# Kernel optimization log

Hardware: AMD Instinct MI355X
Metric: run time of the kernel (lower is better)

Reference implementation:

```python
import jax, jax.numpy as jnp
import numpy as np
import math

B, C, L = 64, 16, 4096
EMB, DEPTH, NEXP = 256, 2, 4
SHAPE, STRIDE = 8, 4
NPATCH = (L - SHAPE) // STRIDE + 1  # 1023
SPARSE = 0.5
NF = 32

def gelu(x):
    return jax.nn.gelu(x, approximate=False)

def conv1d(x, w, stride=1, pad=0):
    return jax.lax.conv_general_dilated(x, w, (stride,), [(pad, pad)],
                                        dimension_numbers=('NCH', 'OIH', 'NCH'))

def rmsnorm(x, g):
    # F.normalize(x, dim=-1) * gamma * sqrt(D)
    n = jnp.sqrt(jnp.sum(x * x, axis=-1, keepdims=True))
    return x / jnp.maximum(n, 1e-12) * g * (x.shape[-1] ** 0.5)

def setup_inputs():
    ks = jax.random.split(jax.random.key(0), 16)
    r = lambda i, s: jax.random.normal(ks[i], s, jnp.float32) * 0.02
    return dict(
        x=jax.random.normal(ks[0], (B, C, L), jnp.float32),
        epoch=100, warm_up=50,
        emb_w=r(1, (EMB, C, SHAPE)), emb_b=jnp.zeros((EMB,), jnp.float32),
        pos_embed=r(2, (1, NPATCH, EMB)),
        attn_w1=r(3, (EMB, 8)), attn_b1=jnp.zeros((8,), jnp.float32),
        attn_w2=r(4, (8, 1)), attn_b2=jnp.zeros((1,), jnp.float32),
        gate_w=r(5, (EMB, NEXP)), gate_b=jnp.zeros((NEXP,), jnp.float32),
        ex_w1=r(6, (NEXP, EMB, EMB)), ex_b1=jnp.zeros((NEXP, EMB), jnp.float32),
        ex_w2=r(7, (NEXP, EMB, EMB)), ex_b2=jnp.zeros((NEXP, EMB), jnp.float32),
        moe_gamma=jnp.ones((EMB,), jnp.float32),
        norm1_g=jnp.ones((DEPTH, EMB), jnp.float32),
        norm2_g=jnp.ones((DEPTH, EMB), jnp.float32),
        bott_w=r(8, (DEPTH, NF, EMB, 1)),
        conv_w39=r(9, (DEPTH, NF, NF, 39)),
        conv_w19=r(10, (DEPTH, NF, NF, 19)),
        conv_w9=r(11, (DEPTH, NF, NF, 9)),
        mp_w=r(12, (DEPTH, NF, EMB, 1)),
        bn_g=jnp.ones((DEPTH, 4 * NF), jnp.float32),
        bn_b=jnp.zeros((DEPTH, 4 * NF), jnp.float32),
        proj_w=r(13, (DEPTH, 4 * NF, EMB)),
        proj_b=jnp.zeros((DEPTH, EMB), jnp.float32),
        head_w=r(14, (EMB, 1)), head_b=jnp.zeros((1,), jnp.float32),
    )

def _forward(x, epoch, warm_up, emb_w, emb_b, pos_embed, attn_w1, attn_b1,
             attn_w2, attn_b2, gate_w, gate_b, ex_w1, ex_b1, ex_w2, ex_b2,
             moe_gamma, norm1_g, norm2_g, bott_w, conv_w39, conv_w19, conv_w9,
             mp_w, bn_g, bn_b, proj_w, proj_b, head_w, head_b):
    def attn(h):  # (B,N,D) -> (B,N,1) sigmoid importance scores
        return jax.nn.sigmoid(jnp.tanh(h @ attn_w1 + attn_b1) @ attn_w2 + attn_b2)

    def moe(h):  # top-1 routed MoE; compute all experts densely, select via one-hot
        Bm, Nm, D = h.shape
        hf = h.reshape(-1, D)  # (T, D)
        logits = jax.nn.softmax(hf @ gate_w + gate_b, axis=-1)  # (T, E)
        top_idx = jnp.argmax(logits, axis=-1)
        top_val = jnp.max(logits, axis=-1, keepdims=True)
        mid = gelu(jnp.einsum('td,edh->eth', hf, ex_w1) + ex_b1[:, None, :])
        ye = jnp.einsum('eth,ehd->etd', mid, ex_w2) + ex_b2[:, None, :]
        sel = jax.nn.one_hot(top_idx, NEXP, dtype=h.dtype)  # (T, E)
        out = jnp.einsum('etd,te->td', ye, sel)
        y = rmsnorm((hf + out * top_val).reshape(Bm, Nm, D), moe_gamma)
        imp = logits.sum(0)
        load = jnp.var(imp, ddof=1) / (imp.mean() ** 2 + 1e-10)
        return gelu(y), load

    def inception(xc, i):  # xc: (B, D, T) -> (B, 4*NF, T)
        xb = conv1d(xc, bott_w[i])  # bottleneck 1x1 -> NF channels
        mp = jax.lax.reduce_window(xc, -jnp.inf, jax.lax.max, (1, 1, 3),
                                   (1, 1, 1), [(0, 0), (0, 0), (1, 1)])
        out = jnp.concatenate([conv1d(xb, conv_w39[i], pad=19),
                               conv1d(xb, conv_w19[i], pad=9),
                               conv1d(xb, conv_w9[i], pad=4),
                               conv1d(mp, mp_w[i])], axis=1)
        # BatchNorm1d eval mode: running mean 0 / var 1, affine gamma/beta
        out = out * (bn_g[i] / np.float32(np.sqrt(1.0 + 1e-5)))[None, :, None] \
              + bn_b[i][None, :, None]
        return gelu(out)

    def incep_branch(h, i):  # (B,N,D) -> (B,N,D)
        io = inception(jnp.transpose(h, (0, 2, 1)), i)
        return jnp.transpose(io, (0, 2, 1)) @ proj_w[i] + proj_b[i]

    h = conv1d(x, emb_w, stride=STRIDE) + emb_b[None, :, None]  # (B, EMB, N)
    h = jnp.transpose(h, (0, 2, 1)) + pos_embed  # N == NPATCH -> no interp
    # pos_drop is identity at inference

    schedule = np.linspace(0.0, SPARSE, DEPTH)
    total_loss = jnp.zeros((), h.dtype)
    end_scores = None
    for i in range(DEPTH):
        ratio = 1.0 if epoch < warm_up else 1.0 - float(schedule[i])
        is_last = (i == DEPTH - 1)
        N = h.shape[1]
        x_n = rmsnorm(h, norm1_g[i])
        scores = attn(x_n)  # (B, N, 1)
        if ratio < 1.0 and N > 2:
            left_k = max(math.ceil(ratio * N), 1)
            xs = x_n * scores
            idx = jnp.sort(jax.lax.top_k(scores[..., 0], left_k)[1], axis=1)
            left_x = jnp.take_along_axis(xs, idx[:, :, None], axis=1)
            # sum of non-topk tokens == total sum minus topk sum
            extra = xs.sum(1, keepdims=True) - left_x.sum(1, keepdims=True)
            h = jnp.concatenate([left_x, extra], axis=1)  # (B, left_k+1, D)
            x_n2 = rmsnorm(h, norm2_g[i])
            moe_out, loss = moe(x_n2)
            h = h + moe_out + incep_branch(x_n2, i)
            total_loss = total_loss + loss
        else:
            h = x_n * scores
            h = h + incep_branch(rmsnorm(h, norm2_g[i]), i)
        if is_last:
            end_scores = attn(h)  # dropout identity; scores on pre-gelu x
        h = gelu(h)
    logits = h @ head_w + head_b  # (B, N', 1)
    cls = (logits * end_scores).mean(axis=1)  # (B, 1)
    return cls[..., 0], total_loss

def reference(x, epoch, warm_up, emb_w, emb_b, pos_embed, attn_w1, attn_b1,
              attn_w2, attn_b2, gate_w, gate_b, ex_w1, ex_b1, ex_w2, ex_b2,
              moe_gamma, norm1_g, norm2_g, bott_w, conv_w39, conv_w19, conv_w9,
              mp_w, bn_g, bn_b, proj_w, proj_b, head_w, head_b):
    return _forward(x, epoch, warm_up, emb_w, emb_b, pos_embed, attn_w1,
                    attn_b1, attn_w2, attn_b2, gate_w, gate_b, ex_w1, ex_b1,
                    ex_w2, ex_b2, moe_gamma, norm1_g, norm2_g, bott_w,
                    conv_w39, conv_w19, conv_w9, mp_w, bn_g, bn_b, proj_w,
                    proj_b, head_w, head_b)
```

## Files before the change

kernel.cpp:

```cpp
#include <hip/hip_runtime.h>
#include <math.h>

#define BB 64
#define EMB 256
#define N0 1023
#define N1 513
#define NTOK0 (BB * N0)
#define NTOK1 (BB * N1)
#define GCH 16

typedef __attribute__((ext_vector_type(8))) short short8;
typedef __attribute__((ext_vector_type(4))) float f32x4;

__device__ __forceinline__ float gelu_f(float x) {
    return 0.5f * x * (1.0f + erff(x * 0.7071067811865476f));
}

__device__ __forceinline__ float4 gelu4(float4 v) {
    return make_float4(gelu_f(v.x), gelu_f(v.y), gelu_f(v.z), gelu_f(v.w));
}

__device__ __forceinline__ float wave_reduce(float v) {
#pragma unroll
    for (int o = 32; o > 0; o >>= 1) v += __shfl_down(v, o, 64);
    return v;
}

__device__ __forceinline__ float attn_finish(float p[8], const float* __restrict__ b1,
                                             const float* __restrict__ w2, float b2v,
                                             int lane) {
#pragma unroll
    for (int o = 1; o <= 4; o <<= 1) {
#pragma unroll
        for (int j = 0; j < 8; j++) p[j] += __shfl_xor(p[j], o, 64);
    }
    int j = lane & 7;
    float a0 = (j & 1) ? p[1] : p[0];
    float a1 = (j & 1) ? p[3] : p[2];
    float a2 = (j & 1) ? p[5] : p[4];
    float a3 = (j & 1) ? p[7] : p[6];
    float c0 = (j & 2) ? a1 : a0;
    float c1 = (j & 2) ? a3 : a2;
    float q  = (j & 4) ? c1 : c0;
#pragma unroll
    for (int o = 8; o <= 32; o <<= 1) q += __shfl_xor(q, o, 64);
    float w = tanhf(q + b1[j]) * w2[j];
#pragma unroll
    for (int o = 1; o <= 4; o <<= 1) w += __shfl_xor(w, o, 64);
    float z = w + b2v;
    return 1.0f / (1.0f + expf(-z));
}

__device__ __forceinline__ unsigned short f2bf(float f) {
    unsigned int u = __float_as_uint(f);
    u = (u + 0x7FFFu + ((u >> 16) & 1u)) >> 16;
    return (unsigned short)u;
}
__device__ __forceinline__ float bf2f(unsigned short h) {
    return __uint_as_float(((unsigned int)h) << 16);
}

__global__ void convert_bf16(const float* __restrict__ ew1, const float* __restrict__ ew2,
                             const float* __restrict__ pjw,
                             const float* __restrict__ cw39, const float* __restrict__ cw19,
                             const float* __restrict__ cw9, const float* __restrict__ embw,
                             const float* __restrict__ bott, const float* __restrict__ mpw,
                             unsigned short* __restrict__ w1t, unsigned short* __restrict__ w2t,
                             unsigned short* __restrict__ pjwb,
                             unsigned short* __restrict__ cwh, unsigned short* __restrict__ cwl,
                             unsigned short* __restrict__ ewh, unsigned short* __restrict__ ewl,
                             unsigned short* __restrict__ bth, unsigned short* __restrict__ btl,
                             unsigned short* __restrict__ mph, unsigned short* __restrict__ mpl,
                             float* __restrict__ imp, int* __restrict__ counts) {
    int idx = blockIdx.x * 256 + threadIdx.x;
    if (blockIdx.x == 0 && threadIdx.x >= 252) {
        int i = threadIdx.x - 252;
        imp[i] = 0.0f; counts[i] = 0;
    }
    if (idx < 262144) {
        int e = idx >> 16, r = idx & 65535, n = r >> 8, k = r & 255;
        w1t[idx] = f2bf(ew1[(e << 16) + (k << 8) + n]);
    } else if (idx < 524288) {
        int j = idx - 262144;
        int e = j >> 16, r = j & 65535, n = r >> 8, k = r & 255;
        w2t[j] = f2bf(ew2[(e << 16) + (k << 8) + n]);
    } else if (idx < 589824) {
        int j = idx - 524288;
        int d = j >> 15, r = j & 32767, n = r >> 7, k = r & 127;
        pjwb[j] = f2bf(pjw[(d << 15) + (k << 8) + n]);
    } else if (idx < 727040) {
        int j = idx - 589824;
        int d = j / 68608, r = j % 68608;
        const float* src; int KT, rr;
        if (r < 39936)      { src = cw39; KT = 39; rr = r; }
        else if (r < 59392) { src = cw19; KT = 19; rr = r - 39936; }
        else                { src = cw9;  KT = 9;  rr = r - 59392; }
        int KK = KT * 32;
        int fo = rr / KK, jj = rr % KK, k = jj >> 5, fi = jj & 31;
        float w = src[(((d * 32 + fo) * 32) + fi) * KT + k];
        unsigned short h = f2bf(w);
        cwh[j] = h;
        cwl[j] = f2bf(w - bf2f(h));
    } else if (idx < 759808) {
        int j = idx - 727040;
        float w = embw[j];
        unsigned short h = f2bf(w);
        ewh[j] = h;
        ewl[j] = f2bf(w - bf2f(h));
    } else if (idx < 776192) {
        int j = idx - 759808;
        float w = bott[j];
        unsigned short h = f2bf(w);
        bth[j] = h;
        btl[j] = f2bf(w - bf2f(h));
    } else if (idx < 792576) {
        int j = idx - 776192;
        float w = mpw[j];
        unsigned short h = f2bf(w);
        mph[j] = h;
        mpl[j] = f2bf(w - bf2f(h));
    }
}

__global__ __launch_bounds__(256, 2)
void embed_mfma(const float* __restrict__ x, const unsigned short* __restrict__ ewh,
                const unsigned short* __restrict__ ewl, const float* __restrict__ emb_b,
                const float* __restrict__ pos, float* __restrict__ A) {
    int b = blockIdx.y;
    int n0 = blockIdx.x * 64;
    __shared__ __align__(16) unsigned short tokh[64 * 128];
    __shared__ __align__(16) unsigned short tokl[64 * 128];
    int tid = threadIdx.x;
#pragma unroll
    for (int it = 0; it < 4; it++) {
        int idx = tid + it * 256;
        int m = idx & 63, c = idx >> 6;
        int tok = n0 + m;
        float v[8] = {0.f, 0.f, 0.f, 0.f, 0.f, 0.f, 0.f, 0.f};
        if (tok < N0) {
            const float* p = x + ((size_t)b * 16 + c) * 4096 + 4 * tok;
            float4 a = *(const float4*)p;
            float4 bq = *(const float4*)(p + 4);
            v[0] = a.x; v[1] = a.y; v[2] = a.z; v[3] = a.w;
            v[4] = bq.x; v[5] = bq.y; v[6] = bq.z; v[7] = bq.w;
        }
        short8 hv, lv;
#pragma unroll
        for (int j = 0; j < 8; j++) {
            unsigned short hh = f2bf(v[j]);
            hv[j] = (short)hh;
            lv[j] = (short)f2bf(v[j] - bf2f(hh));
        }
        int si = (m << 7) + ((c << 3) ^ ((m & 7) << 3));
        *(short8*)(&tokh[si]) = hv;
        *(short8*)(&tokl[si]) = lv;
    }
    __syncthreads();

    int lane = tid & 63, wid = tid >> 6;
    int nb = wid << 6;
    int arow = lane & 15;
    int kgrp = (lane >> 4) << 3;
    int rb = (lane >> 4) << 2;

    f32x4 acc[4][4];
#pragma unroll
    for (int mt = 0; mt < 4; mt++)
#pragma unroll
        for (int nt = 0; nt < 4; nt++) acc[mt][nt] = f32x4{0.f, 0.f, 0.f, 0.f};

    for (int ks = 0; ks < 4; ks++) {
        int kk = (ks << 5) + kgrp;
        short8 ah[4], al[4], bh[4], bl[4];
#pragma unroll
        for (int mt = 0; mt < 4; mt++) {
            int m = (mt << 4) + arow;
            int si = (m << 7) + (kk ^ ((m & 7) << 3));
            ah[mt] = *(const short8*)(&tokh[si]);
            al[mt] = *(const short8*)(&tokl[si]);
        }
#pragma unroll
        for (int nt = 0; nt < 4; nt++) {
            int n = nb + (nt << 4) + arow;
            bh[nt] = *(const short8*)(&ewh[(n << 7) + kk]);
            bl[nt] = *(const short8*)(&ewl[(n << 7) + kk]);
        }
#pragma unroll
        for (int mt = 0; mt < 4; mt++) {
#pragma unroll
            for (int nt = 0; nt < 4; nt++) {
                acc[mt][nt] = __builtin_amdgcn_mfma_f32_16x16x32_bf16(ah[mt], bh[nt], acc[mt][nt], 0, 0, 0);
                acc[mt][nt] = __builtin_amdgcn_mfma_f32_16x16x32_bf16(al[mt], bh[nt], acc[mt][nt], 0, 0, 0);
                acc[mt][nt] = __builtin_amdgcn_mfma_f32_16x16x32_bf16(ah[mt], bl[nt], acc[mt][nt], 0, 0, 0);
            }
        }
    }

    float eb[4];
#pragma unroll
    for (int nt = 0; nt < 4; nt++) eb[nt] = emb_b[nb + (nt << 4) + arow];
#pragma unroll
    for (int mt = 0; mt < 4; mt++) {
#pragma unroll
        for (int nt = 0; nt < 4; nt++) {
            int n = nb + (nt << 4) + arow;
#pragma unroll
            for (int r = 0; r < 4; r++) {
                int m = (mt << 4) + rb + r;
                int tok = n0 + m;
                if (tok < N0)
                    A[((size_t)b * N0 + tok) * 256 + n] =
                        acc[mt][nt][r] + eb[nt] + pos[(size_t)tok * 256 + n];
            }
        }
    }
}

__global__ void norm_attn_kernel(const float* __restrict__ in, float* __restrict__ outv,
                                 float* __restrict__ score_out, const float* __restrict__ g,
                                 const float* __restrict__ w1, const float* __restrict__ b1,
                                 const float* __restrict__ w2, const float* __restrict__ b2,
                                 int scale_out, int pregelu,
                                 float* __restrict__ outv2, const float* __restrict__ g2,
                                 int T) {
    int wid = threadIdx.x >> 6, lane = threadIdx.x & 63;
    int t = blockIdx.x * 4 + wid;
    if (t >= T) return;
    float4 v = ((const float4*)(in + (size_t)t * 256))[lane];
    if (pregelu) v = gelu4(v);
    float4 xn = v;
    if (g != nullptr) {
        float ss = v.x * v.x + v.y * v.y + v.z * v.z + v.w * v.w;
        ss = wave_reduce(ss);
        ss = __shfl(ss, 0, 64);
        float inv = 16.0f / fmaxf(sqrtf(ss), 1e-12f);
        float4 g4 = ((const float4*)g)[lane];
        xn.x = v.x * inv * g4.x; xn.y = v.y * inv * g4.y;
        xn.z = v.z * inv * g4.z; xn.w = v.w * inv * g4.w;
    }
    float p[8];
#pragma unroll
    for (int j = 0; j < 8; j++) p[j] = 0.0f;
    const float xv[4] = {xn.x, xn.y, xn.z, xn.w};
#pragma unroll
    for (int c = 0; c < 4; c++) {
        const float4* wr = (const float4*)(w1 + (4 * lane + c) * 8);
        float4 wa = wr[0], wb = wr[1];
        float xx = xv[c];
        p[0] += xx * wa.x; p[1] += xx * wa.y; p[2] += xx * wa.z; p[3] += xx * wa.w;
        p[4] += xx * wb.x; p[5] += xx * wb.y; p[6] += xx * wb.z; p[7] += xx * wb.w;
    }
    float sc = attn_finish(p, b1, w2, b2[0], lane);
    if (score_out && lane == 0) score_out[t] = sc;
    if (outv) {
        float m = scale_out ? sc : 1.0f;
        float4 o = make_float4(xn.x * m, xn.y * m, xn.z * m, xn.w * m);
        ((float4*)(outv + (size_t)t * 256))[lane] = o;
    }
    if (outv2) {
        float ss2 = xn.x * xn.x + xn.y * xn.y + xn.z * xn.z + xn.w * xn.w;
        ss2 = wave_reduce(ss2);
        ss2 = __shfl(ss2, 0, 64);
        float inv2 = 16.0f / fmaxf(sqrtf(ss2), 1e-12f);
        float4 q4 = ((const float4*)g2)[lane];
        float4 o;
        o.x = xn.x * inv2 * q4.x; o.y = xn.y * inv2 * q4.y;
        o.z = xn.z * inv2 * q4.z; o.w = xn.w * inv2 * q4.w;
        ((float4*)(outv2 + (size_t)t * 256))[lane] = o;
    }
}

__global__ void rmsnorm_kernel(const float* __restrict__ in, float* __restrict__ out,
                               const float* __restrict__ g, int T) {
    int wid = threadIdx.x >> 6, lane = threadIdx.x & 63;
    int t = blockIdx.x * 4 + wid;
    if (t >= T) return;
    float4 v = ((const float4*)(in + (size_t)t * 256))[lane];
    float ss = v.x * v.x + v.y * v.y + v.z * v.z + v.w * v.w;
    ss = wave_reduce(ss);
    ss = __shfl(ss, 0, 64);
    float inv = 16.0f / fmaxf(sqrtf(ss), 1e-12f);
    float4 g4 = ((const float4*)g)[lane];
    float4 o;
    o.x = v.x * inv * g4.x; o.y = v.y * inv * g4.y;
    o.z = v.z * inv * g4.z; o.w = v.w * inv * g4.w;
    ((float4*)(out + (size_t)t * 256))[lane] = o;
}

__global__ __launch_bounds__(256, 2)
void pw_mfma(const float* __restrict__ xn, const unsigned short* __restrict__ bwh,
             const unsigned short* __restrict__ bwl, const unsigned short* __restrict__ mwh,
             const unsigned short* __restrict__ mwl, const float* __restrict__ bng,
             const float* __restrict__ bnb, float* __restrict__ xb,
             float* __restrict__ cat, int N) {
    int b = blockIdx.y;
    int t0 = blockIdx.x * 32;
    __shared__ __align__(16) unsigned short xth[34 * 256];
    __shared__ __align__(16) unsigned short xtl[34 * 256];
    __shared__ __align__(16) unsigned short xmh[32 * 256];
    __shared__ __align__(16) unsigned short xml[32 * 256];
    const float* xbase = xn + (size_t)b * N * 256;
    int tid = threadIdx.x;
    for (int idx = tid; idx < 34 * 32; idx += 256) {
        int r = idx >> 5, p = (idx & 31) << 3;
        int t = t0 - 1 + r;
        short8 hv, lv;
        if (t >= 0 && t < N) {
            const float4* q = (const float4*)(xbase + (size_t)t * 256 + p);
            float4 a = q[0], c = q[1];
            float v[8] = {a.x, a.y, a.z, a.w, c.x, c.y, c.z, c.w};
#pragma unroll
            for (int j = 0; j < 8; j++) {
                unsigned short hh = f2bf(v[j]);
                hv[j] = (short)hh;
                lv[j] = (short)f2bf(v[j] - bf2f(hh));
            }
        } else {
#pragma unroll
            for (int j = 0; j < 8; j++) { hv[j] = (short)0xFF80; lv[j] = 0; }
        }
        int si = (r << 8) + (p ^ ((r & 7) << 3));
        *(short8*)(&xth[si]) = hv;
        *(short8*)(&xtl[si]) = lv;
    }
    __syncthreads();
    for (int idx = tid; idx < 32 * 32; idx += 256) {
        int r = idx >> 5, p = (idx & 31) << 3;
        int s0 = ((r + 0) << 8) + (p ^ (((r + 0) & 7) << 3));
        int s1 = ((r + 1) << 8) + (p ^ (((r + 1) & 7) << 3));
        int s2 = ((r + 2) << 8) + (p ^ (((r + 2) & 7) << 3));
        short8 h0 = *(const short8*)(&xth[s0]), l0 = *(const short8*)(&xtl[s0]);
        short8 h1 = *(const short8*)(&xth[s1]), l1 = *(const short8*)(&xtl[s1]);
        short8 h2 = *(const short8*)(&xth[s2]), l2 = *(const short8*)(&xtl[s2]);
        short8 hv, lv;
#pragma unroll
        for (int j = 0; j < 8; j++) {
            float a = bf2f((unsigned short)h0[j]) + bf2f((unsigned short)l0[j]);
            float c = bf2f((unsigned short)h1[j]) + bf2f((unsigned short)l1[j]);
            float d = bf2f((unsigned short)h2[j]) + bf2f((unsigned short)l2[j]);
            float m = fmaxf(fmaxf(a, c), d);
            unsigned short hh = f2bf(m);
            hv[j] = (short)hh;
            lv[j] = (short)f2bf(m - bf2f(hh));
        }
        int si = (r << 8) + (p ^ ((r & 7) << 3));
        *(short8*)(&xmh[si]) = hv;
        *(short8*)(&xml[si]) = lv;
    }
    __syncthreads();

    int lane = tid & 63, wid = tid >> 6;
    int mt = wid & 1, path = wid >> 1;
    int arow = lane & 15, kgrp = (lane >> 4) << 3, rb = (lane >> 4) << 2;
    const unsigned short* Wh = path ? mwh : bwh;
    const unsigned short* Wl = path ? mwl : bwl;
    f32x4 acc[2];
    acc[0] = f32x4{0.f, 0.f, 0.f, 0.f};
    acc[1] = f32x4{0.f, 0.f, 0.f, 0.f};

    int m = (mt << 4) + arow;
    int rowA = path ? m : (m + 1);
    const unsigned short* Ah = path ? xmh : xth;
    const unsigned short* Al = path ? xml : xtl;
    for (int ks = 0; ks < 8; ks++) {
        int kk = (ks << 5) + kgrp;
        int si = (rowA << 8) + (kk ^ ((rowA & 7) << 3));
        short8 ah = *(const short8*)(&Ah[si]);
        short8 al = *(const short8*)(&Al[si]);
#pragma unroll
        for (int nt = 0; nt < 2; nt++) {
            int n = (nt << 4) + arow;
            short8 bh = *(const short8*)(&Wh[n * 256 + kk]);
            short8 bl = *(const short8*)(&Wl[n * 256 + kk]);
            acc[nt] = __builtin_amdgcn_mfma_f32_16x16x32_bf16(ah, bh, acc[nt], 0, 0, 0);
            acc[nt] = __builtin_amdgcn_mfma_f32_16x16x32_bf16(al, bh, acc[nt], 0, 0, 0);
            acc[nt] = __builtin_amdgcn_mfma_f32_16x16x32_bf16(ah, bl, acc[nt], 0, 0, 0);
        }
    }

    const float BN_DIV = 1.0000050f;
    if (path == 0) {
#pragma unroll
        for (int nt = 0; nt < 2; nt++) {
            int n = (nt << 4) + arow;
#pragma unroll
            for (int r = 0; r < 4; r++) {
                int t = t0 + (mt << 4) + rb + r;
                if (t < N) xb[((size_t)b * N + t) * 32 + n] = acc[nt][r];
            }
        }
    } else {
#pragma unroll
        for (int nt = 0; nt < 2; nt++) {
            int n = (nt << 4) + arow;
            float scl = bng[96 + n] / BN_DIV;
            float sh = bnb[96 + n];
#pragma unroll
            for (int r = 0; r < 4; r++) {
                int t = t0 + (mt << 4) + rb + r;
                if (t < N)
                    cat[((size_t)b * N + t) * 128 + 96 + n] = gelu_f(acc[nt][r] * scl + sh);
            }
        }
    }
}

__global__ __launch_bounds__(256, 2)
void conv_mfma(const float* __restrict__ xb, const unsigned short* __restrict__ wh,
               const unsigned short* __restrict__ wl, const float* __restrict__ bng,
               const float* __restrict__ bnb, float* __restrict__ cat, int N) {
    int b = blockIdx.y;
    int t0 = blockIdx.x * 128;
    __shared__ __align__(16) unsigned short tokh[167 * 32];
    __shared__ __align__(16) unsigned short tokl[167 * 32];
    const float* xbase = xb + (size_t)b * N * 32;
    int tid = threadIdx.x;
    for (int idx = tid; idx < 167 * 16; idx += 256) {
        int r = idx >> 4, c = (idx & 15) << 1;
        int t = t0 - 19 + r;
        float vx = 0.f, vy = 0.f;
        if (t >= 0 && t < N) {
            const float2 v = *(const float2*)(xbase + (size_t)t * 32 + c);
            vx = v.x; vy = v.y;
        }
        unsigned short h0 = f2bf(vx), h1 = f2bf(vy);
        unsigned short l0 = f2bf(vx - bf2f(h0)), l1 = f2bf(vy - bf2f(h1));
        int si = (r << 5) + ((((c >> 3) ^ ((r >> 1) & 3)) << 3) | (c & 7));
        *(unsigned int*)(&tokh[si]) = (unsigned)h0 | ((unsigned)h1 << 16);
        *(unsigned int*)(&tokl[si]) = (unsigned)l0 | ((unsigned)l1 << 16);
    }
    __syncthreads();
    int lane = tid & 63, wid = tid >> 6;
    int arow = lane & 15, g = lane >> 4, kgrp = g << 3;
    int rb = g << 2;
    f32x4 acc[3][2][2];
#pragma unroll
    for (int i = 0; i < 3; i++)
#pragma unroll
        for (int m = 0; m < 2; m++) {
            acc[i][m][0] = f32x4{0.f, 0.f, 0.f, 0.f};
            acc[i][m][1] = f32x4{0.f, 0.f, 0.f, 0.f};
        }

#define SIA(row) (((row) << 5) + ((g ^ (((row) >> 1) & 3)) << 3))
#define CONV_BR(KT, BOFF, WOFF, BR)                                                        \
    {                                                                                      \
        const int KK = (KT) * 32;                                                          \
        int r0 = (WOFF) + wid * 32 + arow;                                                 \
        const unsigned short* whp = wh + (BOFF) + arow * KK + kgrp;                        \
        const unsigned short* wlp = wl + (BOFF) + arow * KK + kgrp;                        \
        for (int k = 0; k < (KT); k++) {                                                   \
            int ra = r0 + k, rc = r0 + 16 + k;                                             \
            short8 ah0 = *(const short8*)(&tokh[SIA(ra)]);                                 \
            short8 al0 = *(const short8*)(&tokl[SIA(ra)]);                                 \
            short8 ah1 = *(const short8*)(&tokh[SIA(rc)]);                                 \
            short8 al1 = *(const short8*)(&tokl[SIA(rc)]);                                 \
            short8 bh0 = *(const short8*)(&whp[k * 32]);                                   \
            short8 bl0 = *(const short8*)(&wlp[k * 32]);                                   \
            short8 bh1 = *(const short8*)(&whp[16 * KK + k * 32]);                         \
            short8 bl1 = *(const short8*)(&wlp[16 * KK + k * 32]);                         \
            acc[BR][0][0] = __builtin_amdgcn_mfma_f32_16x16x32_bf16(ah0, bh0, acc[BR][0][0], 0, 0, 0); \
            acc[BR][0][1] = __builtin_amdgcn_mfma_f32_16x16x32_bf16(ah0, bh1, acc[BR][0][1], 0, 0, 0); \
            acc[BR][0][0] = __builtin_amdgcn_mfma_f32_16x16x32_bf16(al0, bh0, acc[BR][0][0], 0, 0, 0); \
            acc[BR][0][1] = __builtin_amdgcn_mfma_f32_16x16x32_bf16(al0, bh1, acc[BR][0][1], 0, 0, 0); \
            acc[BR][0][0] = __builtin_amdgcn_mfma_f32_16x16x32_bf16(ah0, bl0, acc[BR][0][0], 0, 0, 0); \
            acc[BR][0][1] = __builtin_amdgcn_mfma_f32_16x16x32_bf16(ah0, bl1, acc[BR][0][1], 0, 0, 0); \
            acc[BR][1][0] = __builtin_amdgcn_mfma_f32_16x16x32_bf16(ah1, bh0, acc[BR][1][0], 0, 0, 0); \
            acc[BR][1][1] = __builtin_amdgcn_mfma_f32_16x16x32_bf16(ah1, bh1, acc[BR][1][1], 0, 0, 0); \
            acc[BR][1][0] = __builtin_amdgcn_mfma_f32_16x16x32_bf16(al1, bh0, acc[BR][1][0], 0, 0, 0); \
            acc[BR][1][1] = __builtin_amdgcn_mfma_f32_16x16x32_bf16(al1, bh1, acc[BR][1][1], 0, 0, 0); \
            acc[BR][1][0] = __builtin_amdgcn_mfma_f32_16x16x32_bf16(ah1, bl0, acc[BR][1][0], 0, 0, 0); \
            acc[BR][1][1] = __builtin_amdgcn_mfma_f32_16x16x32_bf16(ah1, bl1, acc[BR][1][1], 0, 0, 0); \
        }                                                                                  \
    }

    CONV_BR(39, 0, 0, 0)
    CONV_BR(19, 39936, 10, 1)
    CONV_BR(9, 59392, 15, 2)
#undef CONV_BR
#undef SIA

    const float BN_DIV = 1.0000050f;
    const int COFFS[3] = {0, 32, 64};
#pragma unroll
    for (int br = 0; br < 3; br++) {
#pragma unroll
        for (int mt = 0; mt < 2; mt++) {
#pragma unroll
            for (int nt = 0; nt < 2; nt++) {
                int fo = COFFS[br] + nt * 16 + arow;
                float scl = bng[fo] / BN_DIV;
                float sh = bnb[fo];
#pragma unroll
                for (int r = 0; r < 4; r++) {
                    int t = t0 + wid * 32 + mt * 16 + rb + r;
                    if (t < N)
                        cat[((size_t)b * N + t) * 128 + fo] =
                            gelu_f(acc[br][mt][nt][r] * scl + sh);
                }
            }
        }
    }
}

__global__ __launch_bounds__(256, 2)
void proj_mfma(const float* __restrict__ cat, const unsigned short* __restrict__ pjt,
               const float* __restrict__ pb, float* __restrict__ A, int TN) {
    int t0 = blockIdx.x * 64;
    __shared__ __align__(16) unsigned short tokh[64 * 128];
    __shared__ __align__(16) unsigned short tokl[64 * 128];
    int tid = threadIdx.x;
#pragma unroll
    for (int it = 0; it < 4; it++) {
        int idx = tid + it * 256;
        int m = idx >> 4, c = idx & 15;
        int t = t0 + m;
        float v[8] = {0.f, 0.f, 0.f, 0.f, 0.f, 0.f, 0.f, 0.f};
        if (t < TN) {
            const float4* q = (const float4*)(cat + (size_t)t * 128 + (c << 3));
            float4 a = q[0], bq = q[1];
            v[0] = a.x; v[1] = a.y; v[2] = a.z; v[3] = a.w;
            v[4] = bq.x; v[5] = bq.y; v[6] = bq.z; v[7] = bq.w;
        }
        short8 hv, lv;
#pragma unroll
        for (int j = 0; j < 8; j++) {
            unsigned short hh = f2bf(v[j]);
            hv[j] = (short)hh;
            lv[j] = (short)f2bf(v[j] - bf2f(hh));
        }
        int si = (m << 7) + ((c << 3) ^ ((m & 7) << 3));
        *(short8*)(&tokh[si]) = hv;
        *(short8*)(&tokl[si]) = lv;
    }
    __syncthreads();

    int lane = tid & 63, wid = tid >> 6;
    int nb = wid << 6;
    int arow = lane & 15;
    int kgrp = (lane >> 4) << 3;
    int rb = (lane >> 4) << 2;

    f32x4 acc[4][4];
#pragma unroll
    for (int mt = 0; mt < 4; mt++)
#pragma unroll
        for (int nt = 0; nt < 4; nt++) acc[mt][nt] = f32x4{0.f, 0.f, 0.f, 0.f};

    for (int ks = 0; ks < 4; ks++) {
        int kk = (ks << 5) + kgrp;
        short8 ah[4], al[4], bw[4];
#pragma unroll
        for (int mt = 0; mt < 4; mt++) {
            int m = (mt << 4) + arow;
            int si = (m << 7) + (kk ^ ((m & 7) << 3));
            ah[mt] = *(const short8*)(&tokh[si]);
            al[mt] = *(const short8*)(&tokl[si]);
        }
#pragma unroll
        for (int nt = 0; nt < 4; nt++) {
            int n = nb + (nt << 4) + arow;
            bw[nt] = *(const short8*)(&pjt[(n << 7) + kk]);
        }
#pragma unroll
        for (int mt = 0; mt < 4; mt++) {
#pragma unroll
            for (int nt = 0; nt < 4; nt++) {
                acc[mt][nt] = __builtin_amdgcn_mfma_f32_16x16x32_bf16(ah[mt], bw[nt], acc[mt][nt], 0, 0, 0);
                acc[mt][nt] = __builtin_amdgcn_mfma_f32_16x16x32_bf16(al[mt], bw[nt], acc[mt][nt], 0, 0, 0);
            }
        }
    }

    float bias[4];
#pragma unroll
    for (int nt = 0; nt < 4; nt++) bias[nt] = pb[nb + (nt << 4) + arow];
#pragma unroll
    for (int mt = 0; mt < 4; mt++) {
#pragma unroll
        for (int nt = 0; nt < 4; nt++) {
            int n = nb + (nt << 4) + arow;
#pragma unroll
            for (int r = 0; r < 4; r++) {
                int t = t0 + (mt << 4) + rb + r;
                if (t < TN) {
                    float* ap = A + (size_t)t * 256 + n;
                    *ap += acc[mt][nt][r] + bias[nt];
                }
            }
        }
    }
}

__global__ __launch_bounds__(1024) void topk_kernel(const float* __restrict__ s,
                                                    int* __restrict__ selpos) {
    int b = blockIdx.x;
    int tid = threadIdx.x;
    __shared__ float srt[1024];
    __shared__ int buf[1024];
    __shared__ int Gtot_s;
    float val = (tid < N0) ? s[(size_t)b * N0 + tid] : -INFINITY;
    srt[tid] = val;
    __syncthreads();
    for (int ksz = 2; ksz <= 1024; ksz <<= 1) {
        for (int j = ksz >> 1; j > 0; j >>= 1) {
            int ixj = tid ^ j;
            if (ixj > tid) {
                float a = srt[tid], c = srt[ixj];
                bool up = ((tid & ksz) == 0);
                if ((a > c) == up) { srt[tid] = c; srt[ixj] = a; }
            }
            __syncthreads();
        }
    }
    float thr = srt[512];
    __syncthreads();
    int isG = (val > thr) ? 1 : 0;
    int isE = (val == thr) ? 1 : 0;
    buf[tid] = isG;
    __syncthreads();
    for (int off = 1; off < 1024; off <<= 1) {
        int cur = buf[tid];
        int add = (tid >= off) ? buf[tid - off] : 0;
        __syncthreads();
        buf[tid] = cur + add;
        __syncthreads();
    }
    if (tid == 0) Gtot_s = buf[1023];
    __syncthreads();
    int Gtot = Gtot_s;
    int Eneed = 512 - Gtot;
    buf[tid] = isE;
    __syncthreads();
    for (int off = 1; off < 1024; off <<= 1) {
        int cur = buf[tid];
        int add = (tid >= off) ? buf[tid - off] : 0;
        __syncthreads();
        buf[tid] = cur + add;
        __syncthreads();
    }
    int eqExcl = buf[tid] - isE;
    int sel = (isG || (isE && eqExcl < Eneed)) ? 1 : 0;
    __syncthreads();
    buf[tid] = sel;
    __syncthreads();
    for (int off = 1; off < 1024; off <<= 1) {
        int cur = buf[tid];
        int add = (tid >= off) ? buf[tid - off] : 0;
        __syncthreads();
        buf[tid] = cur + add;
        __syncthreads();
    }
    int pos = buf[tid] - sel;
    selpos[b * 1024 + tid] = sel ? pos : -1;
}

__global__ void scatter_kernel(const float* __restrict__ xn, const float* __restrict__ s,
                               const int* __restrict__ selpos, float* __restrict__ A,
                               float* __restrict__ part) {
    int b = blockIdx.y;
    int chunk = blockIdx.x;
    int wid = threadIdx.x >> 6, lane = threadIdx.x & 63;
    int t0 = chunk * 64;
    __shared__ float sl[64];
    __shared__ int pl[64];
    if (threadIdx.x < 64) {
        int t = t0 + threadIdx.x;
        sl[threadIdx.x] = (t < N0) ? s[(size_t)b * N0 + t] : 0.0f;
        pl[threadIdx.x] = (t < N0) ? selpos[b * 1024 + t] : -1;
    }
    __syncthreads();
    const float* xbase = xn + ((size_t)b * N0 + t0) * 256;
    float* obase = A + (size_t)b * N1 * 256;
    float4 nonsel = make_float4(0.f, 0.f, 0.f, 0.f);
    int tmax = (t0 + 64 <= N0) ? 64 : (N0 - t0);
    for (int i = wid; i < tmax; i += 4) {
        float sc = sl[i];
        float4 v = ((const float4*)(xbase + (size_t)i * 256))[lane];
        v.x *= sc; v.y *= sc; v.z *= sc; v.w *= sc;
        int p = pl[i];
        if (p >= 0) ((float4*)(obase + (size_t)p * 256))[lane] = v;
        else { nonsel.x += v.x; nonsel.y += v.y; nonsel.z += v.z; nonsel.w += v.w; }
    }
    ((float4*)(part + ((size_t)(b * GCH + chunk) * 4 + wid) * 256))[lane] = nonsel;
}

__global__ void extra_kernel(const float* __restrict__ part, float* __restrict__ A) {
    int b = blockIdx.x, d = threadIdx.x;
    float acc = 0.0f;
    for (int c = 0; c < GCH * 4; c++) acc += part[((size_t)b * GCH * 4 + c) * 256 + d];
    A[((size_t)b * N1 + 512) * 256 + d] = acc;
}

__global__ void gate_kernel(const float* __restrict__ xn2, const float* __restrict__ gw,
                            const float* __restrict__ gb, float* __restrict__ topval,
                            int* __restrict__ buckets, int* __restrict__ counts,
                            float* __restrict__ imp, int T) {
    int tid = threadIdx.x;
    int t = blockIdx.x * 256 + tid;
    __shared__ float4 gws[256];
    __shared__ int lcount[4];
    __shared__ int lbase[4];
    __shared__ float limp[4];
    gws[tid] = ((const float4*)gw)[tid];
    if (tid < 4) { lcount[tid] = 0; limp[tid] = 0.0f; }
    __syncthreads();
    bool valid = (t < T);
    float a0 = 0, a1 = 0, a2 = 0, a3 = 0;
    if (valid) {
        const float4* xb4 = (const float4*)(xn2 + (size_t)t * 256);
#pragma unroll 8
        for (int d4 = 0; d4 < 64; d4++) {
            float4 xv = xb4[d4];
            float4 w0 = gws[4 * d4], w1 = gws[4 * d4 + 1];
            float4 w2 = gws[4 * d4 + 2], w3 = gws[4 * d4 + 3];
            a0 += xv.x * w0.x + xv.y * w1.x + xv.z * w2.x + xv.w * w3.x;
            a1 += xv.x * w0.y + xv.y * w1.y + xv.z * w2.y + xv.w * w3.y;
            a2 += xv.x * w0.z + xv.y * w1.z + xv.z * w2.z + xv.w * w3.z;
            a3 += xv.x * w0.w + xv.y * w1.w + xv.z * w2.w + xv.w * w3.w;
        }
    }
    float q0 = 0, q1 = 0, q2 = 0, q3 = 0;
    int eid = 0;
    int lrank = 0;
    if (valid) {
        float l0 = a0 + gb[0], l1 = a1 + gb[1], l2 = a2 + gb[2], l3 = a3 + gb[3];
        float m = fmaxf(fmaxf(l0, l1), fmaxf(l2, l3));
        float e0 = expf(l0 - m), e1 = expf(l1 - m), e2 = expf(l2 - m), e3 = expf(l3 - m);
        float ssum = e0 + e1 + e2 + e3;
        q0 = e0 / ssum; q1 = e1 / ssum; q2 = e2 / ssum; q3 = e3 / ssum;
        float bv = q0;
        if (q1 > bv) { bv = q1; eid = 1; }
        if (q2 > bv) { bv = q2; eid = 2; }
        if (q3 > bv) { bv = q3; eid = 3; }
        topval[t] = bv;
        lrank = atomicAdd(&lcount[eid], 1);
    }
    float r0 = wave_reduce(q0), r1 = wave_reduce(q1);
    float r2 = wave_reduce(q2), r3 = wave_reduce(q3);
    if ((tid & 63) == 0) {
        atomicAdd(&limp[0], r0); atomicAdd(&limp[1], r1);
        atomicAdd(&limp[2], r2); atomicAdd(&limp[3], r3);
    }
    __syncthreads();
    if (tid < 4) {
        lbase[tid] = atomicAdd(&counts[tid], lcount[tid]);
        atomicAdd(&imp[tid], limp[tid]);
    }
    __syncthreads();
    if (valid) buckets[eid * T + lbase[eid] + lrank] = t;
}

__global__ __launch_bounds__(512, 1)
void ffn_kernel(const float* __restrict__ xn2, const unsigned short* __restrict__ w1t,
                const float* __restrict__ b1, const unsigned short* __restrict__ w2t,
                const float* __restrict__ b2, const float* __restrict__ topval,
                const int* __restrict__ buckets, const int* __restrict__ counts,
                float* __restrict__ C, int T) {
    int e = blockIdx.y;
    int cnt = counts[e];
    int base = blockIdx.x * 32;
    if (base >= cnt) return;
    __shared__ __align__(16) unsigned short tokh[32 * 256];
    __shared__ __align__(16) unsigned short tokl[32 * 256];
    __shared__ int tids[32];
    __shared__ float tv[32];
    int tid = threadIdx.x;
    if (tid < 32) {
        int idx = base + tid;
        int t = (idx < cnt) ? buckets[e * T + idx] : -1;
        tids[tid] = t;
        tv[tid] = (t >= 0) ? topval[t] : 0.0f;
    }
    __syncthreads();
#pragma unroll
    for (int it = 0; it < 2; it++) {
        int cc = tid + it * 512;
        int m = cc >> 5, d0 = (cc & 31) << 3;
        int t = tids[m];
        float4 a = make_float4(0.f, 0.f, 0.f, 0.f), b = a;
        if (t >= 0) {
            const float4* p = (const float4*)(xn2 + (size_t)t * 256 + d0);
            a = p[0]; b = p[1];
        }
        float v[8] = {a.x, a.y, a.z, a.w, b.x, b.y, b.z, b.w};
        short8 hv, lv;
#pragma unroll
        for (int j = 0; j < 8; j++) {
            unsigned short hh = f2bf(v[j]);
            hv[j] = (short)hh;
            lv[j] = (short)f2bf(v[j] - bf2f(hh));
        }
        int si = (m << 8) + (d0 ^ ((m & 7) << 3));
        *(short8*)(&tokh[si]) = hv;
        *(short8*)(&tokl[si]) = lv;
    }
    __syncthreads();

    int lane = tid & 63, wid = tid >> 6;
    int nb = wid << 5;
    int arow = lane & 15;
    int kgrp = (lane >> 4) << 3;
    int rb = (lane >> 4) << 2;
    const unsigned short* W1 = w1t + ((size_t)e << 16);
    const unsigned short* W2 = w2t + ((size_t)e << 16);

    f32x4 acc[2][2];
#pragma unroll
    for (int mt = 0; mt < 2; mt++)
#pragma unroll
        for (int nt = 0; nt < 2; nt++) acc[mt][nt] = f32x4{0.f, 0.f, 0.f, 0.f};

#define FFN_KLOOP32(WPTR)                                                                  \
    for (int ks = 0; ks < 8; ks++) {                                                       \
        int kk = (ks << 5) + kgrp;                                                         \
        short8 ah[2], al[2], bw[2];                                                        \
        _Pragma("unroll")                                                                  \
        for (int mt = 0; mt < 2; mt++) {                                                   \
            int m = (mt << 4) + arow;                                                      \
            int si = (m << 8) + (kk ^ ((m & 7) << 3));                                     \
            ah[mt] = *(const short8*)(&tokh[si]);                                          \
            al[mt] = *(const short8*)(&tokl[si]);                                          \
        }                                                                                  \
        _Pragma("unroll")                                                                  \
        for (int nt = 0; nt < 2; nt++)                                                     \
            bw[nt] = *(const short8*)(&WPTR[((size_t)(nb + (nt << 4) + arow) << 8) + kk]); \
        _Pragma("unroll")                                                                  \
        for (int mt = 0; mt < 2; mt++) {                                                   \
            _Pragma("unroll")                                                              \
            for (int nt = 0; nt < 2; nt++) {                                               \
                acc[mt][nt] = __builtin_amdgcn_mfma_f32_16x16x32_bf16(                     \
                    ah[mt], bw[nt], acc[mt][nt], 0, 0, 0);                                 \
                acc[mt][nt] = __builtin_amdgcn_mfma_f32_16x16x32_bf16(                     \
                    al[mt], bw[nt], acc[mt][nt], 0, 0, 0);                                 \
            }                                                                              \
        }                                                                                  \
    }

    FFN_KLOOP32(W1)

    float b1v[2];
#pragma unroll
    for (int nt = 0; nt < 2; nt++) b1v[nt] = b1[(e << 8) + nb + (nt << 4) + arow];
    __syncthreads();
#pragma unroll
    for (int mt = 0; mt < 2; mt++) {
#pragma unroll
        for (int nt = 0; nt < 2; nt++) {
            int kd = nb + (nt << 4) + arow;
#pragma unroll
            for (int r = 0; r < 4; r++) {
                int m = (mt << 4) + rb + r;
                float mid = gelu_f(acc[mt][nt][r] + b1v[nt]);
                unsigned short hh = f2bf(mid);
                int si = (m << 8) + (kd ^ ((m & 7) << 3));
                tokh[si] = hh;
                tokl[si] = f2bf(mid - bf2f(hh));
            }
        }
    }
    __syncthreads();

#pragma unroll
    for (int mt = 0; mt < 2; mt++)
#pragma unroll
        for (int nt = 0; nt < 2; nt++) acc[mt][nt] = f32x4{0.f, 0.f, 0.f, 0.f};

    FFN_KLOOP32(W2)
#undef FFN_KLOOP32

    float b2v[2];
#pragma unroll
    for (int nt = 0; nt < 2; nt++) b2v[nt] = b2[(e << 8) + nb + (nt << 4) + arow];
#pragma unroll
    for (int mt = 0; mt < 2; mt++) {
        int tt[4]; float tvv[4];
#pragma unroll
        for (int r = 0; r < 4; r++) {
            int m = (mt << 4) + rb + r;
            tt[r] = tids[m];
            tvv[r] = tv[m];
        }
#pragma unroll
        for (int nt = 0; nt < 2; nt++) {
            int n = nb + (nt << 4) + arow;
#pragma unroll
            for (int r = 0; r < 4; r++) {
                int t = tt[r];
                if (t >= 0) {
                    float val = acc[mt][nt][r] + b2v[nt];
                    C[(size_t)t * 256 + n] =
                        xn2[(size_t)t * 256 + n] + val * tvv[r];
                }
            }
        }
    }
}

__global__ void moe_add_kernel(const float* __restrict__ C, float* __restrict__ A,
                               const float* __restrict__ gamma, int T) {
    int wid = threadIdx.x >> 6, lane = threadIdx.x & 63;
    int t = blockIdx.x * 4 + wid;
    if (t >= T) return;
    float4 v = ((const float4*)(C + (size_t)t * 256))[lane];
    float ss = v.x * v.x + v.y * v.y + v.z * v.z + v.w * v.w;
    ss = wave_reduce(ss);
    ss = __shfl(ss, 0, 64);
    float inv = 16.0f / fmaxf(sqrtf(ss), 1e-12f);
    float4 g4 = ((const float4*)gamma)[lane];
    float4* ap = (float4*)(A + (size_t)t * 256) + lane;
    float4 a = *ap;
    a.x += gelu_f(v.x * inv * g4.x); a.y += gelu_f(v.y * inv * g4.y);
    a.z += gelu_f(v.z * inv * g4.z); a.w += gelu_f(v.w * inv * g4.w);
    *ap = a;
}

__global__ void endhead_kernel(const float* __restrict__ A, const float* __restrict__ w1,
                               const float* __restrict__ b1, const float* __restrict__ w2,
                               const float* __restrict__ b2, const float* __restrict__ hw,
                               const float* __restrict__ hb, float* __restrict__ contrib,
                               int T) {
    int wid = threadIdx.x >> 6, lane = threadIdx.x & 63;
    int t = blockIdx.x * 4 + wid;
    if (t >= T) return;
    float4 v = ((const float4*)(A + (size_t)t * 256))[lane];
    float p[8];
#pragma unroll
    for (int j = 0; j < 8; j++) p[j] = 0.0f;
    const float xv[4] = {v.x, v.y, v.z, v.w};
#pragma unroll
    for (int c = 0; c < 4; c++) {
        const float4* wr = (const float4*)(w1 + (4 * lane + c) * 8);
        float4 wa = wr[0], wb = wr[1];
        float xx = xv[c];
        p[0] += xx * wa.x; p[1] += xx * wa.y; p[2] += xx * wa.z; p[3] += xx * wa.w;
        p[4] += xx * wb.x; p[5] += xx * wb.y; p[6] += xx * wb.z; p[7] += xx * wb.w;
    }
    float4 h4 = ((const float4*)hw)[lane];
    float hp = gelu_f(v.x) * h4.x + gelu_f(v.y) * h4.y + gelu_f(v.z) * h4.z + gelu_f(v.w) * h4.w;
    hp = wave_reduce(hp);
    float sc = attn_finish(p, b1, w2, b2[0], lane);
    if (lane == 0) {
        contrib[t] = (hp + hb[0]) * sc * (1.0f / (float)N1);
    }
}

__global__ void finalsum_kernel(const float* __restrict__ contrib,
                                const float* __restrict__ imp, float* __restrict__ out) {
    int b = blockIdx.x, tid = threadIdx.x;
    __shared__ float red[4];
    const float* cb = contrib + (size_t)b * N1;
    float v = cb[tid] + cb[256 + tid];
    if (tid == 0) v += cb[512];
    float s = wave_reduce(v);
    int wid = tid >> 6, lane = tid & 63;
    if (lane == 0) red[wid] = s;
    __syncthreads();
    if (tid == 0) {
        out[b] = red[0] + red[1] + red[2] + red[3];
        if (b == 0) {
            float i0 = imp[0], i1 = imp[1], i2 = imp[2], i3 = imp[3];
            float mean = (i0 + i1 + i2 + i3) * 0.25f;
            float var = ((i0 - mean) * (i0 - mean) + (i1 - mean) * (i1 - mean) +
                         (i2 - mean) * (i2 - mean) + (i3 - mean) * (i3 - mean)) / 3.0f;
            out[64] = var / (mean * mean + 1e-10f);
        }
    }
}

extern "C" void kernel_launch(void* const* d_in, const int* in_sizes, int n_in,
                              void* d_out, int out_size, void* d_ws, size_t ws_size,
                              hipStream_t stream) {
    const float* x    = (const float*)d_in[0];
    const float* embw = (const float*)d_in[3];
    const float* embb = (const float*)d_in[4];
    const float* pos  = (const float*)d_in[5];
    const float* aw1  = (const float*)d_in[6];
    const float* ab1  = (const float*)d_in[7];
    const float* aw2  = (const float*)d_in[8];
    const float* ab2  = (const float*)d_in[9];
    const float* gw   = (const float*)d_in[10];
    const float* gb   = (const float*)d_in[11];
    const float* ew1  = (const float*)d_in[12];
    const float* eb1  = (const float*)d_in[13];
    const float* ew2  = (const float*)d_in[14];
    const float* eb2  = (const float*)d_in[15];
    const float* mg   = (const float*)d_in[16];
    const float* n1g  = (const float*)d_in[17];
    const float* n2g  = (const float*)d_in[18];
    const float* bott = (const float*)d_in[19];
    const float* cw39 = (const float*)d_in[20];
    const float* cw19 = (const float*)d_in[21];
    const float* cw9  = (const float*)d_in[22];
    const float* mpw  = (const float*)d_in[23];
    const float* bng  = (const float*)d_in[24];
    const float* bnb  = (const float*)d_in[25];
    const float* pjw  = (const float*)d_in[26];
    const float* pjb  = (const float*)d_in[27];
    const float* hw   = (const float*)d_in[28];
    const float* hb   = (const float*)d_in[29];
    float* out = (float*)d_out;

    float* W = (float*)d_ws;
    size_t off = 0;
    auto alloc = [&](size_t n) { float* p = W + off; off += n; return p; };
    float* A    = alloc((size_t)NTOK0 * 256);
    float* Bb   = alloc((size_t)NTOK0 * 256);
    float* CD   = alloc((size_t)NTOK1 * 256);
    float* XB   = alloc((size_t)NTOK0 * 32);
    float* sS   = alloc(NTOK0);
    float* ctb  = alloc(NTOK1);
    float* tval = alloc(NTOK1);
    float* imp  = alloc(4);
    float* part = alloc((size_t)BB * GCH * 4 * 256);
    off = (off + 3) & ~(size_t)3;
    unsigned short* w1t  = (unsigned short*)(W + off); off += 262144 / 2;
    unsigned short* w2t  = (unsigned short*)(W + off); off += 262144 / 2;
    unsigned short* pjwb = (unsigned short*)(W + off); off += 65536 / 2;
    unsigned short* cwh  = (unsigned short*)(W + off); off += 137216 / 2;
    unsigned short* cwl  = (unsigned short*)(W + off); off += 137216 / 2;
    unsigned short* ewh  = (unsigned short*)(W + off); off += 32768 / 2;
    unsigned short* ewl  = (unsigned short*)(W + off); off += 32768 / 2;
    unsigned short* bth  = (unsigned short*)(W + off); off += 16384 / 2;
    unsigned short* btl  = (unsigned short*)(W + off); off += 16384 / 2;
    unsigned short* mph  = (unsigned short*)(W + off); off += 16384 / 2;
    unsigned short* mpl  = (unsigned short*)(W + off); off += 16384 / 2;
    int* selpos  = (int*)(W + off); off += (size_t)BB * 1024;
    int* buckets = (int*)(W + off); off += (size_t)4 * NTOK1;
    int* counts  = (int*)(W + off); off += 4;

    convert_bf16<<<3096, 256, 0, stream>>>(ew1, ew2, pjw, cw39, cw19, cw9, embw, bott, mpw,
                                           w1t, w2t, pjwb, cwh, cwl, ewh, ewl,
                                           bth, btl, mph, mpl, imp, counts);

    embed_mfma<<<dim3(16, BB), 256, 0, stream>>>(x, ewh, ewl, embb, pos, A);
    norm_attn_kernel<<<NTOK0 / 4, 256, 0, stream>>>(A, A, nullptr, n1g, aw1, ab1, aw2, ab2,
                                                    1, 0, Bb, n2g, NTOK0);
    pw_mfma<<<dim3(32, BB), 256, 0, stream>>>(Bb, bth, btl, mph, mpl, bng, bnb, XB, CD, N0);
    conv_mfma<<<dim3(8, BB), 256, 0, stream>>>(XB, cwh, cwl, bng, bnb, CD, N0);
    proj_mfma<<<NTOK0 / 64, 256, 0, stream>>>(CD, pjwb, pjb, A, NTOK0);

    norm_attn_kernel<<<NTOK0 / 4, 256, 0, stream>>>(A, Bb, sS, n1g + 256, aw1, ab1, aw2, ab2,
                                                    0, 1, nullptr, nullptr, NTOK0);
    topk_kernel<<<BB, 1024, 0, stream>>>(sS, selpos);
    scatter_kernel<<<dim3(GCH, BB), 256, 0, stream>>>(Bb, sS, selpos, A, part);
    extra_kernel<<<BB, 256, 0, stream>>>(part, A);
    rmsnorm_kernel<<<NTOK1 / 4, 256, 0, stream>>>(A, Bb, n2g + 256, NTOK1);
    gate_kernel<<<(NTOK1 + 255) / 256, 256, 0, stream>>>(Bb, gw, gb, tval, buckets, counts, imp,
                                                         NTOK1);
    ffn_kernel<<<dim3((NTOK1 + 31) / 32, 4), 512, 0, stream>>>(Bb, w1t, eb1, w2t, eb2, tval,
                                                               buckets, counts, CD, NTOK1);
    moe_add_kernel<<<NTOK1 / 4, 256, 0, stream>>>(CD, A, mg, NTOK1);
    pw_mfma<<<dim3((N1 + 31) / 32, BB), 256, 0, stream>>>(Bb, bth + 8192, btl + 8192,
                                                          mph + 8192, mpl + 8192,
                                                          bng + 128, bnb + 128, XB, CD, N1);
    conv_mfma<<<dim3((N1 + 127) / 128, BB), 256, 0, stream>>>(XB, cwh + 68608, cwl + 68608,
                                                              bng + 128, bnb + 128, CD, N1);
    proj_mfma<<<NTOK1 / 64, 256, 0, stream>>>(CD, pjwb + 32768, pjb + 256, A, NTOK1);
    endhead_kernel<<<NTOK1 / 4, 256, 0, stream>>>(A, aw1, ab1, aw2, ab2, hw, hb, ctb, NTOK1);
    finalsum_kernel<<<BB, 256, 0, stream>>>(ctb, imp, out);
}
```

Measured before the change: 733.7 us.

## Fold rmsnorm into pointwise conv loader and scatter, drop intermediate buffer writes

The layer-0 second rmsnorm moves into pw_mfma. The kernel computes per-row sums of squares in a first pass over the tile, then scales while converting to bf16 hi/lo, so norm_attn no longer writes a normalized copy. The layer-1 gelu, rmsnorm and score scaling move into scatter_kernel, so norm_attn no longer writes the normalized tensor Bb. Buffer roles A and Bb are swapped downstream to match. This cuts full-tensor HBM writes and reads, at the cost of reading input rows twice in pw_mfma and doing redundant norm work on halo rows.

```diff
diff --git a/kernel.cpp b/kernel.cpp
--- a/kernel.cpp
+++ b/kernel.cpp
@@ -288,7 +288,8 @@
 }
 
 __global__ __launch_bounds__(256, 2)
-void pw_mfma(const float* __restrict__ xn, const unsigned short* __restrict__ bwh,
+void pw_mfma(const float* __restrict__ xn, const float* __restrict__ nrm_g,
+             const unsigned short* __restrict__ bwh,
              const unsigned short* __restrict__ bwl, const unsigned short* __restrict__ mwh,
              const unsigned short* __restrict__ mwl, const float* __restrict__ bng,
              const float* __restrict__ bnb, float* __restrict__ xb,
@@ -299,8 +300,30 @@
     __shared__ __align__(16) unsigned short xtl[34 * 256];
     __shared__ __align__(16) unsigned short xmh[32 * 256];
     __shared__ __align__(16) unsigned short xml[32 * 256];
+    __shared__ float ssrow[34];
+    __shared__ float invrow[34];
     const float* xbase = xn + (size_t)b * N * 256;
     int tid = threadIdx.x;
+    if (nrm_g) {
+        for (int idx = tid; idx < 34 * 32; idx += 256) {
+            int r = idx >> 5, p = (idx & 31) << 3;
+            int t = t0 - 1 + r;
+            float ssp = 0.0f;
+            if (t >= 0 && t < N) {
+                const float4* q = (const float4*)(xbase + (size_t)t * 256 + p);
+                float4 a = q[0], c = q[1];
+                ssp = a.x * a.x + a.y * a.y + a.z * a.z + a.w * a.w +
+                      c.x * c.x + c.y * c.y + c.z * c.z + c.w * c.w;
+            }
+#pragma unroll
+            for (int o = 1; o <= 16; o <<= 1) ssp += __shfl_xor(ssp, o, 64);
+            if ((tid & 31) == 0) ssrow[r] = ssp;
+        }
+        __syncthreads();
+        for (int r2 = tid; r2 < 34; r2 += 256)
+            invrow[r2] = 16.0f / fmaxf(sqrtf(ssrow[r2]), 1e-12f);
+        __syncthreads();
+    }
     for (int idx = tid; idx < 34 * 32; idx += 256) {
         int r = idx >> 5, p = (idx & 31) << 3;
         int t = t0 - 1 + r;
@@ -309,6 +332,13 @@
             const float4* q = (const float4*)(xbase + (size_t)t * 256 + p);
             float4 a = q[0], c = q[1];
             float v[8] = {a.x, a.y, a.z, a.w, c.x, c.y, c.z, c.w};
+            if (nrm_g) {
+                float iv = invrow[r];
+                const float4* gg = (const float4*)(nrm_g + p);
+                float4 g0 = gg[0], g1 = gg[1];
+                v[0] *= iv * g0.x; v[1] *= iv * g0.y; v[2] *= iv * g0.z; v[3] *= iv * g0.w;
+                v[4] *= iv * g1.x; v[5] *= iv * g1.y; v[6] *= iv * g1.z; v[7] *= iv * g1.w;
+            }
 #pragma unroll
             for (int j = 0; j < 8; j++) {
                 unsigned short hh = f2bf(v[j]);
@@ -655,8 +685,9 @@
     selpos[b * 1024 + tid] = sel ? pos : -1;
 }
 
-__global__ void scatter_kernel(const float* __restrict__ xn, const float* __restrict__ s,
-                               const int* __restrict__ selpos, float* __restrict__ A,
+__global__ void scatter_kernel(const float* __restrict__ xn, const float* __restrict__ gam,
+                               const float* __restrict__ s,
+                               const int* __restrict__ selpos, float* __restrict__ dest,
                                float* __restrict__ part) {
     int b = blockIdx.y;
     int chunk = blockIdx.x;
@@ -671,13 +702,19 @@
     }
     __syncthreads();
     const float* xbase = xn + ((size_t)b * N0 + t0) * 256;
-    float* obase = A + (size_t)b * N1 * 256;
+    float* obase = dest + (size_t)b * N1 * 256;
+    float4 g4 = ((const float4*)gam)[lane];
     float4 nonsel = make_float4(0.f, 0.f, 0.f, 0.f);
     int tmax = (t0 + 64 <= N0) ? 64 : (N0 - t0);
     for (int i = wid; i < tmax; i += 4) {
-        float sc = sl[i];
         float4 v = ((const float4*)(xbase + (size_t)i * 256))[lane];
-        v.x *= sc; v.y *= sc; v.z *= sc; v.w *= sc;
+        v = gelu4(v);
+        float ss = v.x * v.x + v.y * v.y + v.z * v.z + v.w * v.w;
+        ss = wave_reduce(ss);
+        ss = __shfl(ss, 0, 64);
+        float inv = 16.0f / fmaxf(sqrtf(ss), 1e-12f);
+        float m = sl[i] * inv;
+        v.x *= m * g4.x; v.y *= m * g4.y; v.z *= m * g4.z; v.w *= m * g4.w;
         int p = pl[i];
         if (p >= 0) ((float4*)(obase + (size_t)p * 256))[lane] = v;
         else { nonsel.x += v.x; nonsel.y += v.y; nonsel.z += v.z; nonsel.w += v.w; }
@@ -685,11 +722,11 @@
     ((float4*)(part + ((size_t)(b * GCH + chunk) * 4 + wid) * 256))[lane] = nonsel;
 }
 
-__global__ void extra_kernel(const float* __restrict__ part, float* __restrict__ A) {
+__global__ void extra_kernel(const float* __restrict__ part, float* __restrict__ dest) {
     int b = blockIdx.x, d = threadIdx.x;
     float acc = 0.0f;
     for (int c = 0; c < GCH * 4; c++) acc += part[((size_t)b * GCH * 4 + c) * 256 + d];
-    A[((size_t)b * N1 + 512) * 256 + d] = acc;
+    dest[((size_t)b * N1 + 512) * 256 + d] = acc;
 }
 
 __global__ void gate_kernel(const float* __restrict__ xn2, const float* __restrict__ gw,
@@ -897,7 +934,7 @@
     }
 }
 
-__global__ void moe_add_kernel(const float* __restrict__ C, float* __restrict__ A,
+__global__ void moe_add_kernel(const float* __restrict__ C, float* __restrict__ dest,
                                const float* __restrict__ gamma, int T) {
     int wid = threadIdx.x >> 6, lane = threadIdx.x & 63;
     int t = blockIdx.x * 4 + wid;
@@ -908,7 +945,7 @@
     ss = __shfl(ss, 0, 64);
     float inv = 16.0f / fmaxf(sqrtf(ss), 1e-12f);
     float4 g4 = ((const float4*)gamma)[lane];
-    float4* ap = (float4*)(A + (size_t)t * 256) + lane;
+    float4* ap = (float4*)(dest + (size_t)t * 256) + lane;
     float4 a = *ap;
     a.x += gelu_f(v.x * inv * g4.x); a.y += gelu_f(v.y * inv * g4.y);
     a.z += gelu_f(v.z * inv * g4.z); a.w += gelu_f(v.w * inv * g4.w);
@@ -1035,28 +1072,28 @@
 
     embed_mfma<<<dim3(16, BB), 256, 0, stream>>>(x, ewh, ewl, embb, pos, A);
     norm_attn_kernel<<<NTOK0 / 4, 256, 0, stream>>>(A, A, nullptr, n1g, aw1, ab1, aw2, ab2,
-                                                    1, 0, Bb, n2g, NTOK0);
-    pw_mfma<<<dim3(32, BB), 256, 0, stream>>>(Bb, bth, btl, mph, mpl, bng, bnb, XB, CD, N0);
+                                                    1, 0, nullptr, nullptr, NTOK0);
+    pw_mfma<<<dim3(32, BB), 256, 0, stream>>>(A, n2g, bth, btl, mph, mpl, bng, bnb, XB, CD, N0);
     conv_mfma<<<dim3(8, BB), 256, 0, stream>>>(XB, cwh, cwl, bng, bnb, CD, N0);
     proj_mfma<<<NTOK0 / 64, 256, 0, stream>>>(CD, pjwb, pjb, A, NTOK0);
 
-    norm_attn_kernel<<<NTOK0 / 4, 256, 0, stream>>>(A, Bb, sS, n1g + 256, aw1, ab1, aw2, ab2,
-                                                    0, 1, nullptr, nullptr, NTOK0);
+    norm_attn_kernel<<<NTOK0 / 4, 256, 0, stream>>>(A, nullptr, sS, n1g + 256, aw1, ab1,
+                                                    aw2, ab2, 0, 1, nullptr, nullptr, NTOK0);
     topk_kernel<<<BB, 1024, 0, stream>>>(sS, selpos);
-    scatter_kernel<<<dim3(GCH, BB), 256, 0, stream>>>(Bb, sS, selpos, A, part);
-    extra_kernel<<<BB, 256, 0, stream>>>(part, A);
-    rmsnorm_kernel<<<NTOK1 / 4, 256, 0, stream>>>(A, Bb, n2g + 256, NTOK1);
-    gate_kernel<<<(NTOK1 + 255) / 256, 256, 0, stream>>>(Bb, gw, gb, tval, buckets, counts, imp,
+    scatter_kernel<<<dim3(GCH, BB), 256, 0, stream>>>(A, n1g + 256, sS, selpos, Bb, part);
+    extra_kernel<<<BB, 256, 0, stream>>>(part, Bb);
+    rmsnorm_kernel<<<NTOK1 / 4, 256, 0, stream>>>(Bb, A, n2g + 256, NTOK1);
+    gate_kernel<<<(NTOK1 + 255) / 256, 256, 0, stream>>>(A, gw, gb, tval, buckets, counts, imp,
                                                          NTOK1);
-    ffn_kernel<<<dim3((NTOK1 + 31) / 32, 4), 512, 0, stream>>>(Bb, w1t, eb1, w2t, eb2, tval,
+    ffn_kernel<<<dim3((NTOK1 + 31) / 32, 4), 512, 0, stream>>>(A, w1t, eb1, w2t, eb2, tval,
                                                                buckets, counts, CD, NTOK1);
-    moe_add_kernel<<<NTOK1 / 4, 256, 0, stream>>>(CD, A, mg, NTOK1);
-    pw_mfma<<<dim3((N1 + 31) / 32, BB), 256, 0, stream>>>(Bb, bth + 8192, btl + 8192,
+    moe_add_kernel<<<NTOK1 / 4, 256, 0, stream>>>(CD, Bb, mg, NTOK1);
+    pw_mfma<<<dim3((N1 + 31) / 32, BB), 256, 0, stream>>>(A, nullptr, bth + 8192, btl + 8192,
                                                           mph + 8192, mpl + 8192,
                                                           bng + 128, bnb + 128, XB, CD, N1);
     conv_mfma<<<dim3((N1 + 127) / 128, BB), 256, 0, stream>>>(XB, cwh + 68608, cwl + 68608,
                                                               bng + 128, bnb + 128, CD, N1);
-    proj_mfma<<<NTOK1 / 64, 256, 0, stream>>>(CD, pjwb + 32768, pjb + 256, A, NTOK1);
-    endhead_kernel<<<NTOK1 / 4, 256, 0, stream>>>(A, aw1, ab1, aw2, ab2, hw, hb, ctb, NTOK1);
+    proj_mfma<<<NTOK1 / 64, 256, 0, stream>>>(CD, pjwb + 32768, pjb + 256, Bb, NTOK1);
+    endhead_kernel<<<NTOK1 / 4, 256, 0, stream>>>(Bb, aw1, ab1, aw2, ab2, hw, hb, ctb, NTOK1);
     finalsum_kernel<<<BB, 256, 0, stream>>>(ctb, imp, out);
 }
```

Measured after the change: 756.4 us. 3.1% more time.
